# Kernel optimization log

Measured on AMD Instinct MI355X. Metric: run time of the kernel, lower is better.

The kernel has to match this reference:

```python
import jax, jax.numpy as jnp
import numpy as np

N = 100000
E = 3200000
N_IN = 512
N_OUT = 256


def setup_inputs() -> dict:
    key = jax.random.key(0)
    k = jax.random.split(key, 6)
    stdv = 1.0 / np.sqrt(N_IN)
    x = jax.random.normal(k[0], (N, N_IN), dtype=jnp.float32)
    adj_rows = jax.random.randint(k[1], (E,), 0, N, dtype=jnp.int32)
    adj_cols = jax.random.randint(k[2], (E,), 0, N, dtype=jnp.int32)
    adj_vals = jax.random.uniform(k[3], (E,), dtype=jnp.float32)
    W = jax.random.uniform(k[4], (N_OUT, N_IN), minval=-stdv, maxval=stdv, dtype=jnp.float32)
    b = jax.random.uniform(k[5], (N_OUT,), minval=-stdv, maxval=stdv, dtype=jnp.float32)
    return {"x": x, "adj_rows": adj_rows, "adj_cols": adj_cols, "adj_vals": adj_vals, "W": W, "b": b}


def reference(x, adj_rows, adj_cols, adj_vals, W, b):
    # linear projection: x @ W^T + b  -> [N, n_out]
    h = jnp.einsum('ni,oi->no', x, W) + b
    # spmm: out[r] = sum_e adj_vals[e] * h[adj_cols[e]] for edges with row r
    msgs = h[adj_cols] * adj_vals[:, None]          # [E, n_out]
    out = jax.ops.segment_sum(msgs, adj_rows, num_segments=N)
    return out
```

## Files before the change

### kernel.cpp

```cpp
#include <hip/hip_runtime.h>

#define NIN 512
#define NOUT 256
#define NPART 8
#define RPB 32
#define BSH 5
#define CHUNK 2048
#define CSH 11
#define SEG 256
#define SEGSH 8
#define SCAT 1024

typedef __attribute__((ext_vector_type(8))) __bf16 bf16x8;
typedef __attribute__((ext_vector_type(4))) float f32x4;
typedef __attribute__((ext_vector_type(8))) float f32x8;
typedef __attribute__((ext_vector_type(2))) int i32x2;
typedef __attribute__((ext_vector_type(8))) ushort u16x8;

__device__ __forceinline__ ushort f2bf(float f) {
  uint u = __builtin_bit_cast(uint, f);
  uint r = (u + 0x7FFFu + ((u >> 16) & 1u)) >> 16;
  return (ushort)r;
}
__device__ __forceinline__ uint pk2(float a, float b) {
  return (uint)f2bf(a) | ((uint)f2bf(b) << 16);
}
__device__ __forceinline__ float bf2f(ushort u) {
  return __builtin_bit_cast(float, (uint)u << 16);
}

__global__ __launch_bounds__(256) void init_cur_kernel(int* __restrict__ cur,
                                                       int NB) {
  int i = blockIdx.x * 256 + threadIdx.x;
  if (i < NPART * NB) {
    int s = i / NB;
    int b = i - s * NB;
    cur[i] = ((b << 3) + s) << SEGSH;
  }
}

__global__ __launch_bounds__(512) void gemm_scatter_kernel(
    const float* __restrict__ x, const float* __restrict__ W,
    const float* __restrict__ bias, ushort* __restrict__ h, int M,
    const int* __restrict__ rows, const int* __restrict__ cols,
    const float* __restrict__ vals, int* __restrict__ cur,
    int2* __restrict__ bufE, int E, int NB, int nchunks, int G) {
  __shared__ ushort a_lds[128 * 40];
  __shared__ ushort b_lds[256 * 40];

  const int t = threadIdx.x;

  if (blockIdx.x >= G) {
    const int s = blockIdx.x & (NPART - 1);
    const int j = (int)blockIdx.x - G;
    const int m = j >> 3;
    const int nres = SCAT >> 3;
    int* mycur = cur + s * NB;
    for (int k = m;; k += nres) {
      int c = k * NPART + s;
      if (c >= nchunks) break;
      int i0 = c << CSH;
      int i1 = min(E, i0 + CHUNK);
      for (int i = i0 + t; i < i1; i += 1024) {
        int ib = i + 512;
        bool hb = ib < i1;
        int r0 = __builtin_nontemporal_load(&rows[i]);
        int c0 = __builtin_nontemporal_load(&cols[i]);
        float v0 = __builtin_nontemporal_load(&vals[i]);
        int r1 = 0, c1 = 0;
        float v1 = 0.f;
        if (hb) {
          r1 = __builtin_nontemporal_load(&rows[ib]);
          c1 = __builtin_nontemporal_load(&cols[ib]);
          v1 = __builtin_nontemporal_load(&vals[ib]);
        }
        int pos0 = atomicAdd(&mycur[r0 >> BSH], 1);
        int pos1 = hb ? atomicAdd(&mycur[r1 >> BSH], 1) : 0;
        int2 p0;
        p0.x = ((r0 & (RPB - 1)) << 17) | c0;
        p0.y = __builtin_bit_cast(int, v0);
        bufE[pos0] = p0;
        if (hb) {
          int2 p1;
          p1.x = ((r1 & (RPB - 1)) << 17) | c1;
          p1.y = __builtin_bit_cast(int, v1);
          bufE[pos1] = p1;
        }
      }
    }
    return;
  }

  const int l = t & 63;
  const int wv = t >> 6;
  const int wr = wv >> 2;
  const int wc = wv & 3;
  const int m0 = blockIdx.x * 128;

  const int lrow = l & 15;
  const int lk = (l >> 4) * 8;

  f32x4 acc[4][4];
#pragma unroll
  for (int i = 0; i < 4; ++i)
#pragma unroll
    for (int j = 0; j < 4; ++j) acc[i][j] = (f32x4){0.f, 0.f, 0.f, 0.f};

  float biasr[4];
#pragma unroll
  for (int j = 0; j < 4; ++j) biasr[j] = bias[wc * 64 + j * 16 + lrow];

  const int arow = t >> 2;
  const int akc = (t & 3) * 8;
  const int brow = t >> 1;
  const int bkc = (t & 1) * 16;

  const bool avalid = (m0 + arow < M);
  const float* xbase = x + (size_t)(m0 + arow) * NIN + akc;
  const float* wbase = W + (size_t)brow * NIN + bkc;

  float4 xa = make_float4(0.f, 0.f, 0.f, 0.f), xb = xa;
  if (avalid) {
    const float4* xs = reinterpret_cast<const float4*>(xbase);
    xa = xs[0];
    xb = xs[1];
  }
  float4 w0, w1, w2, w3;
  {
    const float4* ws = reinterpret_cast<const float4*>(wbase);
    w0 = ws[0]; w1 = ws[1]; w2 = ws[2]; w3 = ws[3];
  }

  for (int kk = 0; kk < 16; ++kk) {
    const int k0 = kk * 32;
    {
      uint4 p;
      p.x = pk2(xa.x, xa.y); p.y = pk2(xa.z, xa.w);
      p.z = pk2(xb.x, xb.y); p.w = pk2(xb.z, xb.w);
      *reinterpret_cast<uint4*>(&a_lds[arow * 40 + akc]) = p;
    }
    {
      uint4 p0, p1;
      p0.x = pk2(w0.x, w0.y); p0.y = pk2(w0.z, w0.w);
      p0.z = pk2(w1.x, w1.y); p0.w = pk2(w1.z, w1.w);
      p1.x = pk2(w2.x, w2.y); p1.y = pk2(w2.z, w2.w);
      p1.z = pk2(w3.x, w3.y); p1.w = pk2(w3.z, w3.w);
      *reinterpret_cast<uint4*>(&b_lds[brow * 40 + bkc]) = p0;
      *reinterpret_cast<uint4*>(&b_lds[brow * 40 + bkc + 8]) = p1;
    }
    __syncthreads();

    if (kk < 15) {
      if (avalid) {
        const float4* xs = reinterpret_cast<const float4*>(xbase + k0 + 32);
        xa = xs[0];
        xb = xs[1];
      }
      const float4* ws = reinterpret_cast<const float4*>(wbase + k0 + 32);
      w0 = ws[0]; w1 = ws[1]; w2 = ws[2]; w3 = ws[3];
    }

    bf16x8 af[4], bf_[4];
#pragma unroll
    for (int i = 0; i < 4; ++i)
      af[i] = *reinterpret_cast<const bf16x8*>(
          &a_lds[(wr * 64 + i * 16 + lrow) * 40 + lk]);
#pragma unroll
    for (int j = 0; j < 4; ++j)
      bf_[j] = *reinterpret_cast<const bf16x8*>(
          &b_lds[(wc * 64 + j * 16 + lrow) * 40 + lk]);
#pragma unroll
    for (int i = 0; i < 4; ++i)
#pragma unroll
      for (int j = 0; j < 4; ++j)
        acc[i][j] = __builtin_amdgcn_mfma_f32_16x16x32_bf16(af[i], bf_[j],
                                                            acc[i][j], 0, 0, 0);
    __syncthreads();
  }

#pragma unroll
  for (int i = 0; i < 4; ++i) {
    const int mbase = m0 + wr * 64 + i * 16 + (l >> 4) * 4;
#pragma unroll
    for (int r = 0; r < 4; ++r) {
      int m = mbase + r;
      if (m >= M) continue;
#pragma unroll
      for (int j = 0; j < 4; ++j)
        h[(size_t)m * NOUT + wc * 64 + j * 16 + lrow] =
            f2bf(acc[i][j][r] + biasr[j]);
    }
  }
}

__global__ __launch_bounds__(256) void bucket_reduce_kernel(
    const ushort* __restrict__ h, const int2* __restrict__ bufE,
    const int* __restrict__ cur, float* __restrict__ out, int M, int NB) {
  __shared__ int2 sbuf[NPART * SEG];
  __shared__ int cnt[RPB];
  __shared__ int off[RPB + 1];
  __shared__ int segn[NPART];

  const int b = blockIdx.x;
  const int t = threadIdx.x;

  if (t < NPART)
    segn[t] = min(cur[t * NB + b] - (((b << 3) + t) << SEGSH), SEG);
  if (t < RPB) cnt[t] = 0;
  __syncthreads();

  int2 ed[NPART];
#pragma unroll
  for (int s = 0; s < NPART; ++s) {
    int2 p = make_int2(0, 0);
    if (t < segn[s]) {
      i32x2 raw = __builtin_nontemporal_load(reinterpret_cast<const i32x2*>(
          &bufE[(size_t)(((b << 3) + s) << SEGSH) + t]));
      p.x = raw.x;
      p.y = raw.y;
      atomicAdd(&cnt[(uint)p.x >> 17], 1);
    }
    ed[s] = p;
  }
  __syncthreads();
  if (t == 0) {
    int run = 0;
#pragma unroll
    for (int j = 0; j < RPB; ++j) { off[j] = run; run += cnt[j]; }
    off[RPB] = run;
  }
  __syncthreads();
  if (t < RPB) cnt[t] = off[t];
  __syncthreads();
#pragma unroll
  for (int s = 0; s < NPART; ++s) {
    if (t < segn[s]) {
      int pos = atomicAdd(&cnt[(uint)ed[s].x >> 17], 1);
      sbuf[pos] = ed[s];
    }
  }
  __syncthreads();

  const int wv = t >> 6;
  const int lane = t & 63;
  const int half = lane >> 5;
  const int hl = lane & 31;
  for (int q = 0; q < 8; ++q) {
    int j = wv * 8 + q;
    int row = b * RPB + j;
    if (row >= M) break;
    int e = off[j];
    const int e1 = off[j + 1];
    f32x8 acc = (f32x8){0.f, 0.f, 0.f, 0.f, 0.f, 0.f, 0.f, 0.f};
    for (; e + 15 < e1; e += 16) {
      u16x8 hv[8];
      float vv[8];
#pragma unroll
      for (int u = 0; u < 8; ++u) {
        int2 p = sbuf[e + 2 * u + half];
        vv[u] = __builtin_bit_cast(float, p.y);
        hv[u] = *reinterpret_cast<const u16x8*>(
            h + (size_t)(p.x & 0x1FFFF) * NOUT + hl * 8);
      }
#pragma unroll
      for (int u = 0; u < 8; ++u)
#pragma unroll
        for (int c = 0; c < 8; ++c) acc[c] += vv[u] * bf2f(hv[u][c]);
    }
    for (; e + 7 < e1; e += 8) {
      u16x8 hv[4];
      float vv[4];
#pragma unroll
      for (int u = 0; u < 4; ++u) {
        int2 p = sbuf[e + 2 * u + half];
        vv[u] = __builtin_bit_cast(float, p.y);
        hv[u] = *reinterpret_cast<const u16x8*>(
            h + (size_t)(p.x & 0x1FFFF) * NOUT + hl * 8);
      }
#pragma unroll
      for (int u = 0; u < 4; ++u)
#pragma unroll
        for (int c = 0; c < 8; ++c) acc[c] += vv[u] * bf2f(hv[u][c]);
    }
    for (; e + 1 < e1; e += 2) {
      int2 p = sbuf[e + half];
      float v = __builtin_bit_cast(float, p.y);
      u16x8 hv = *reinterpret_cast<const u16x8*>(
          h + (size_t)(p.x & 0x1FFFF) * NOUT + hl * 8);
#pragma unroll
      for (int c = 0; c < 8; ++c) acc[c] += v * bf2f(hv[c]);
    }
    if (e < e1) {
      int2 p = sbuf[e];
      float v = half ? 0.f : __builtin_bit_cast(float, p.y);
      u16x8 hv = *reinterpret_cast<const u16x8*>(
          h + (size_t)(p.x & 0x1FFFF) * NOUT + hl * 8);
#pragma unroll
      for (int c = 0; c < 8; ++c) acc[c] += v * bf2f(hv[c]);
    }
#pragma unroll
    for (int c = 0; c < 8; ++c) acc[c] += __shfl(acc[c], hl + 32);
    if (half == 0) {
      f32x4 lo = (f32x4){acc[0], acc[1], acc[2], acc[3]};
      f32x4 hi = (f32x4){acc[4], acc[5], acc[6], acc[7]};
      f32x4* dst = reinterpret_cast<f32x4*>(out + (size_t)row * NOUT + hl * 8);
      __builtin_nontemporal_store(lo, dst);
      __builtin_nontemporal_store(hi, dst + 1);
    }
  }
}

extern "C" void kernel_launch(void* const* d_in, const int* in_sizes, int n_in,
                              void* d_out, int out_size, void* d_ws, size_t ws_size,
                              hipStream_t stream) {
  const float* x        = (const float*)d_in[0];
  const int*   adj_rows = (const int*)d_in[1];
  const int*   adj_cols = (const int*)d_in[2];
  const float* adj_vals = (const float*)d_in[3];
  const float* W        = (const float*)d_in[4];
  const float* b        = (const float*)d_in[5];
  float* out = (float*)d_out;

  const int M = in_sizes[0] / NIN;
  const int E = in_sizes[1];

  const int NB = (M + RPB - 1) >> BSH;
  const int nchunks = (E + CHUNK - 1) >> CSH;

  ushort* h    = (ushort*)d_ws;
  int2*   bufE = (int2*)(h + (size_t)M * NOUT);
  int*    cur  = (int*)(bufE + (size_t)NB * NPART * SEG);

  const int G = (M + 127) / 128;

  init_cur_kernel<<<(NPART * NB + 255) / 256, 256, 0, stream>>>(cur, NB);
  gemm_scatter_kernel<<<G + SCAT, 512, 0, stream>>>(
      x, W, b, h, M, adj_rows, adj_cols, adj_vals, cur, bufE, E, NB, nchunks, G);
  bucket_reduce_kernel<<<NB, 256, 0, stream>>>(h, bufE, cur, out, M, NB);
}
```

Measured before the change: 424.3 us.

## Split bucket reduce into CSR sort and column-sliced gather kernels

The fused bucket-reduce kernel is split in two. A sort kernel writes row-sorted edges and per-row offsets back to global memory. A gather kernel then launches eight blocks per bucket, each covering a 32-column slice of h, with 16 edge groups per wave reduced through xor shuffles. This gives eight times more blocks and short gather segments for better parallelism and L2 locality. The cost is an extra launch, a global round trip for the sorted edges, and each edge record being read eight times.

```diff
diff --git a/kernel.cpp b/kernel.cpp
--- a/kernel.cpp
+++ b/kernel.cpp
@@ -193,9 +193,9 @@
   }
 }
 
-__global__ __launch_bounds__(256) void bucket_reduce_kernel(
-    const ushort* __restrict__ h, const int2* __restrict__ bufE,
-    const int* __restrict__ cur, float* __restrict__ out, int M, int NB) {
+__global__ __launch_bounds__(256) void csr_sort_kernel(
+    int2* __restrict__ bufE, const int* __restrict__ cur,
+    int* __restrict__ rowOff, int NB) {
   __shared__ int2 sbuf[NPART * SEG];
   __shared__ int cnt[RPB];
   __shared__ int off[RPB + 1];
@@ -211,16 +211,16 @@
 
   int2 ed[NPART];
 #pragma unroll
-  for (int s = 0; s < NPART; ++s) {
+  for (int sp = 0; sp < NPART; ++sp) {
     int2 p = make_int2(0, 0);
-    if (t < segn[s]) {
+    if (t < segn[sp]) {
       i32x2 raw = __builtin_nontemporal_load(reinterpret_cast<const i32x2*>(
-          &bufE[(size_t)(((b << 3) + s) << SEGSH) + t]));
+          &bufE[(size_t)(((b << 3) + sp) << SEGSH) + t]));
       p.x = raw.x;
       p.y = raw.y;
       atomicAdd(&cnt[(uint)p.x >> 17], 1);
     }
-    ed[s] = p;
+    ed[sp] = p;
   }
   __syncthreads();
   if (t == 0) {
@@ -233,77 +233,66 @@
   if (t < RPB) cnt[t] = off[t];
   __syncthreads();
 #pragma unroll
-  for (int s = 0; s < NPART; ++s) {
-    if (t < segn[s]) {
-      int pos = atomicAdd(&cnt[(uint)ed[s].x >> 17], 1);
-      sbuf[pos] = ed[s];
-    }
-  }
+  for (int sp = 0; sp < NPART; ++sp) {
+    if (t < segn[sp]) {
+      int pos = atomicAdd(&cnt[(uint)ed[sp].x >> 17], 1);
+      sbuf[pos] = ed[sp];
+    }
+  }
+  __syncthreads();
+
+  const size_t bbase = (size_t)b << 11;
+  const int n = off[RPB];
+#pragma unroll
+  for (int k = 0; k < NPART; ++k) {
+    int i = t + k * 256;
+    if (i < n) bufE[bbase + i] = sbuf[i];
+  }
+  if (t <= RPB) rowOff[b * (RPB + 1) + t] = off[t];
+}
+
+__global__ __launch_bounds__(256) void slice_gather_kernel(
+    const ushort* __restrict__ h, const int2* __restrict__ bufE,
+    const int* __restrict__ rowOff, float* __restrict__ out, int M, int NB) {
+  __shared__ int off[RPB + 1];
+
+  const int bs = blockIdx.x;
+  const int b = bs >> 3;
+  const int s = bs & (NPART - 1);
+  const int t = threadIdx.x;
+
+  if (t <= RPB) off[t] = rowOff[b * (RPB + 1) + t];
   __syncthreads();
 
   const int wv = t >> 6;
   const int lane = t & 63;
-  const int half = lane >> 5;
-  const int hl = lane & 31;
+  const int eg = lane >> 2;
+  const int cg = lane & 3;
+  const int choff = s * 32 + cg * 8;
+  const size_t bbase = (size_t)b << 11;
+
   for (int q = 0; q < 8; ++q) {
-    int j = wv * 8 + q;
-    int row = b * RPB + j;
+    const int j = wv * 8 + q;
+    const int row = b * RPB + j;
     if (row >= M) break;
-    int e = off[j];
     const int e1 = off[j + 1];
     f32x8 acc = (f32x8){0.f, 0.f, 0.f, 0.f, 0.f, 0.f, 0.f, 0.f};
-    for (; e + 15 < e1; e += 16) {
-      u16x8 hv[8];
-      float vv[8];
-#pragma unroll
-      for (int u = 0; u < 8; ++u) {
-        int2 p = sbuf[e + 2 * u + half];
-        vv[u] = __builtin_bit_cast(float, p.y);
-        hv[u] = *reinterpret_cast<const u16x8*>(
-            h + (size_t)(p.x & 0x1FFFF) * NOUT + hl * 8);
-      }
-#pragma unroll
-      for (int u = 0; u < 8; ++u)
-#pragma unroll
-        for (int c = 0; c < 8; ++c) acc[c] += vv[u] * bf2f(hv[u][c]);
-    }
-    for (; e + 7 < e1; e += 8) {
-      u16x8 hv[4];
-      float vv[4];
-#pragma unroll
-      for (int u = 0; u < 4; ++u) {
-        int2 p = sbuf[e + 2 * u + half];
-        vv[u] = __builtin_bit_cast(float, p.y);
-        hv[u] = *reinterpret_cast<const u16x8*>(
-            h + (size_t)(p.x & 0x1FFFF) * NOUT + hl * 8);
-      }
-#pragma unroll
-      for (int u = 0; u < 4; ++u)
-#pragma unroll
-        for (int c = 0; c < 8; ++c) acc[c] += vv[u] * bf2f(hv[u][c]);
-    }
-    for (; e + 1 < e1; e += 2) {
-      int2 p = sbuf[e + half];
-      float v = __builtin_bit_cast(float, p.y);
+    for (int e = off[j] + eg; e < e1; e += 16) {
+      int2 p = bufE[bbase + e];
+      float vv = __builtin_bit_cast(float, p.y);
       u16x8 hv = *reinterpret_cast<const u16x8*>(
-          h + (size_t)(p.x & 0x1FFFF) * NOUT + hl * 8);
-#pragma unroll
-      for (int c = 0; c < 8; ++c) acc[c] += v * bf2f(hv[c]);
-    }
-    if (e < e1) {
-      int2 p = sbuf[e];
-      float v = half ? 0.f : __builtin_bit_cast(float, p.y);
-      u16x8 hv = *reinterpret_cast<const u16x8*>(
-          h + (size_t)(p.x & 0x1FFFF) * NOUT + hl * 8);
-#pragma unroll
-      for (int c = 0; c < 8; ++c) acc[c] += v * bf2f(hv[c]);
-    }
-#pragma unroll
-    for (int c = 0; c < 8; ++c) acc[c] += __shfl(acc[c], hl + 32);
-    if (half == 0) {
+          h + (size_t)(p.x & 0x1FFFF) * NOUT + choff);
+#pragma unroll
+      for (int c = 0; c < 8; ++c) acc[c] += vv * bf2f(hv[c]);
+    }
+#pragma unroll
+    for (int mask = 4; mask <= 32; mask <<= 1)
+#pragma unroll
+      for (int c = 0; c < 8; ++c) acc[c] += __shfl_xor(acc[c], mask);
+    if (eg == 0) {
       f32x4 lo = (f32x4){acc[0], acc[1], acc[2], acc[3]};
       f32x4 hi = (f32x4){acc[4], acc[5], acc[6], acc[7]};
-      f32x4* dst = reinterpret_cast<f32x4*>(out + (size_t)row * NOUT + hl * 8);
+      f32x4* dst = reinterpret_cast<f32x4*>(out + (size_t)row * NOUT + choff);
       __builtin_nontemporal_store(lo, dst);
       __builtin_nontemporal_store(hi, dst + 1);
     }
@@ -330,11 +319,14 @@
   ushort* h    = (ushort*)d_ws;
   int2*   bufE = (int2*)(h + (size_t)M * NOUT);
   int*    cur  = (int*)(bufE + (size_t)NB * NPART * SEG);
+  int*    rowOff = cur + NPART * NB;
 
   const int G = (M + 127) / 128;
 
   init_cur_kernel<<<(NPART * NB + 255) / 256, 256, 0, stream>>>(cur, NB);
   gemm_scatter_kernel<<<G + SCAT, 512, 0, stream>>>(
       x, W, b, h, M, adj_rows, adj_cols, adj_vals, cur, bufE, E, NB, nchunks, G);
-  bucket_reduce_kernel<<<NB, 256, 0, stream>>>(h, bufE, cur, out, M, NB);
-}
+  csr_sort_kernel<<<NB, 256, 0, stream>>>(bufE, cur, rowOff, NB);
+  slice_gather_kernel<<<NB * NPART, 256, 0, stream>>>(h, bufE, rowOff, out, M,
+                                                      NB);
+}
```

New measurement: 570.7 us. 1.34x slower.
